# Performance work log

Measured on AMD Instinct MI355X. Metric: run time of the kernel, lower is better.

Reference implementation:

```python
import jax, jax.numpy as jnp
import numpy as np

# module hyper-params (from NLSearch __init__ defaults)
K = 7        # top-k neighbors
PS = 7       # patch size
WS = 8       # search window (ws x ws candidates)
NHEADS = 1
STRIDE0 = 4  # query grid stride
STRIDE1 = 1  # candidate stride within window


def _reflect(i, n):
    # reflect (mirror) out-of-range indices into [0, n)
    i = jnp.where(i < 0, -i, i)
    return jnp.where(i >= n, 2 * (n - 1) - i, i)


def setup_inputs() -> dict:
    key = jax.random.key(0)
    k0, k1 = jax.random.split(key)
    vid0 = jax.random.normal(k0, (1, 3, 32, 256, 256), dtype=jnp.float32)
    vid1 = jax.random.normal(k1, (1, 3, 32, 256, 256), dtype=jnp.float32)
    return {"vid0": vid0, "vid1": vid1}


def _nl_search(vid0, vid1):
    B, T, C, H, W = vid0.shape
    HD = NHEADS
    c = C // HD
    v0 = vid0.reshape(B, T, HD, c, H, W)
    v1 = vid1.reshape(B, T, HD, c, H, W)
    nH = (H - 1) // STRIDE0 + 1
    nW = (W - 1) // STRIDE0 + 1
    qh = jnp.arange(nH) * STRIDE0  # query centers
    qw = jnp.arange(nW) * STRIDE0
    poff = jnp.arange(PS) - PS // 2  # centered patch offsets

    def patches(v, hc, wc):
        # gather reflect-bounded ps x ps patches centered at (hc, wc)
        hi = _reflect(hc[:, None] + poff[None, :], H)  # [nH, PS]
        wi = _reflect(wc[:, None] + poff[None, :], W)  # [nW, PS]
        p = v[:, :, :, :, hi]          # [B,T,HD,c,nH,PS,W]
        p = p[:, :, :, :, :, :, wi]    # [B,T,HD,c,nH,PS,nW,PS]
        return p

    p0 = patches(v0, qh, qw)  # query patches, reused across all shifts
    woff = (jnp.arange(WS) - WS // 2) * STRIDE1
    shifts = jnp.stack(jnp.meshgrid(woff, woff, indexing='ij'), -1).reshape(-1, 2)  # [WS*WS,2]

    def body(carry, s):
        def step(s_):
            p1 = patches(v1, qh + s_[0], qw + s_[1])
            # patch inner product ('prod' search distance)
            return jnp.einsum('bthcnivj,bthcnivj->bthnv', p0, p1)
        return carry, jax.checkpoint(step)(s)

    _, dists = jax.lax.scan(body, 0, shifts)   # [L,B,T,HD,nH,nW]
    dists = jnp.moveaxis(dists, 0, -1)         # [B,T,HD,nH,nW,L]

    # anchor_self: force the self (zero-shift) candidate to rank first,
    # but return its true distance (bump only used for ordering)
    self_idx = (WS // 2) * WS + (WS // 2)
    adj = dists.at[..., self_idx].add(jnp.asarray(1e30, dists.dtype))
    _, top_idx = jax.lax.top_k(adj, K)                       # [B,T,HD,nH,nW,K]
    top_d = jnp.take_along_axis(dists, top_idx, axis=-1)     # [B,T,HD,nH,nW,K]

    # decode flat shift index -> absolute (t,h,w) neighbor coordinates
    dh = (top_idx // WS - WS // 2) * STRIDE1
    dw = (top_idx % WS - WS // 2) * STRIDE1
    hh = _reflect(qh[None, None, None, :, None, None] + dh, H)
    ww = _reflect(qw[None, None, None, None, :, None] + dw, W)
    tt = jnp.broadcast_to(jnp.arange(T)[None, :, None, None, None, None], hh.shape)
    inds = jnp.stack([tt, hh, ww], -1)  # [B,T,HD,nH,nW,K,3]

    Q = T * nH * nW
    dists_out = jnp.transpose(top_d, (0, 2, 1, 3, 4, 5)).reshape(B, HD, Q, K)
    inds_out = jnp.transpose(inds, (0, 2, 1, 3, 4, 5, 6)).reshape(B, HD, Q, K, 3)
    return dists_out, inds_out


def reference(vid0, vid1):
    return _nl_search(vid0, vid1)
```

## Files before the change

### kernel.cpp

```cpp
#include <hip/hip_runtime.h>

#define TT 3
#define CCH 32
#define HH 256
#define WW 256
#define KK 7
#define NQ 64
#define QPB 16
#define V1W 80
#define V1N (14*V1W)
#define V1P (V1N + 8)
#define V0W 72
#define V0N (7*V0W)
#define V0P (V0N + 16)
#define CHC 4

__device__ __forceinline__ int refl(int i, int n) {
    i = i < 0 ? -i : i;
    return i >= n ? 2*(n-1) - i : i;
}

__global__ __launch_bounds__(256, 4)
void nls_kernel(const float* __restrict__ vid0, const float* __restrict__ vid1,
                float* __restrict__ out) {
    __shared__ float v1s[CHC * V1P];
    __shared__ float v0s[CHC * V0P];

    const int bx  = blockIdx.x;
    const int t   = bx >> 8;
    const int rem = bx & 255;
    const int qy  = rem >> 2;
    const int q0  = (rem & 3) * QPB;
    const int qh  = qy * 4;
    const int w0  = 4*q0 - 7;

    const int tid   = threadIdx.x;
    const int qwi   = tid & 15;
    const int clane = (tid >> 4) & 3;
    const int shq   = tid >> 6;

    int off1[5];
#pragma unroll
    for (int k = 0; k < 5; ++k) {
        int idx = tid + 256*k;
        if (idx < V1N) {
            int r = idx / V1W, wi = idx - r*V1W;
            off1[k] = refl(qh + r - 7, HH) * WW + refl(w0 + wi, WW);
        } else off1[k] = 0;
    }
    int off0[2];
#pragma unroll
    for (int k = 0; k < 2; ++k) {
        int idx = tid + 256*k;
        if (idx < V0N) {
            int r = idx / V0W, wi = idx - r*V0W;
            off0[k] = refl(qh + r - 3, HH) * WW + refl(w0 + wi, WW);
        } else off0[k] = 0;
    }

    float acc[2][8];
#pragma unroll
    for (int l = 0; l < 2; ++l)
#pragma unroll
        for (int b = 0; b < 8; ++b) acc[l][b] = 0.f;

    const float* g0 = vid0 + (size_t)t * (CCH*HH*WW);
    const float* g1 = vid1 + (size_t)t * (CCH*HH*WW);

#pragma unroll 1
    for (int s = 0; s < 8; ++s) {
        const int cb = CHC * s * (HH*WW);
        __syncthreads();
        float t1[CHC][5];
        float t0v[CHC][2];
#pragma unroll
        for (int ch = 0; ch < CHC; ++ch) {
            const float* p1 = g1 + cb + ch*(HH*WW);
            const float* p0 = g0 + cb + ch*(HH*WW);
#pragma unroll
            for (int k = 0; k < 4; ++k) t1[ch][k] = p1[off1[k]];
            t1[ch][4]  = (tid < V1N - 1024) ? p1[off1[4]] : 0.f;
            t0v[ch][0] = p0[off0[0]];
            t0v[ch][1] = (tid < V0N - 256) ? p0[off0[1]] : 0.f;
        }
#pragma unroll
        for (int ch = 0; ch < CHC; ++ch) {
#pragma unroll
            for (int k = 0; k < 4; ++k) v1s[ch*V1P + tid + 256*k] = t1[ch][k];
            if (tid < V1N - 1024) v1s[ch*V1P + tid + 1024] = t1[ch][4];
            v0s[ch*V0P + tid] = t0v[ch][0];
            if (tid < V0N - 256) v0s[ch*V0P + tid + 256] = t0v[ch][1];
        }
        __syncthreads();

        float x[7][8];
        const float* xb = &v0s[clane*V0P + 4*qwi + 4];
#pragma unroll
        for (int i = 0; i < 7; ++i) {
            float4 a = *(const float4*)(xb + i*V0W);
            float4 b = *(const float4*)(xb + i*V0W + 4);
            x[i][0]=a.x; x[i][1]=a.y; x[i][2]=a.z; x[i][3]=a.w;
            x[i][4]=b.x; x[i][5]=b.y; x[i][6]=b.z; x[i][7]=b.w;
        }
        const float* yb = &v1s[clane*V1P + (2*shq)*V1W + 4*qwi];
#pragma unroll
        for (int rr = 0; rr < 8; ++rr) {
            const float4* py = (const float4*)(yb + rr*V1W);
            float4 A = py[0], B = py[1], C = py[2], D = py[3];
            float y[16];
            y[0]=A.x;  y[1]=A.y;  y[2]=A.z;  y[3]=A.w;
            y[4]=B.x;  y[5]=B.y;  y[6]=B.z;  y[7]=B.w;
            y[8]=C.x;  y[9]=C.y;  y[10]=C.z; y[11]=C.w;
            y[12]=D.x; y[13]=D.y; y[14]=D.z; y[15]=D.w;
            if (rr < 7) {
#pragma unroll
                for (int sw = 0; sw < 8; ++sw)
#pragma unroll
                    for (int j = 0; j < 7; ++j)
                        acc[0][sw] += x[rr][j] * y[sw + j];
            }
            if (rr >= 1) {
#pragma unroll
                for (int sw = 0; sw < 8; ++sw)
#pragma unroll
                    for (int j = 0; j < 7; ++j)
                        acc[1][sw] += x[rr-1][j] * y[sw + j];
            }
        }
    }

#pragma unroll
    for (int m = 16; m <= 32; m <<= 1)
#pragma unroll
        for (int l = 0; l < 2; ++l)
#pragma unroll
            for (int b = 0; b < 8; ++b)
                acc[l][b] += __shfl_xor(acc[l][b], m, 64);

    __syncthreads();
    float* dlds = v1s;
    if (clane == 0) {
#pragma unroll
        for (int l = 0; l < 2; ++l)
#pragma unroll
            for (int b = 0; b < 8; ++b)
                dlds[qwi*64 + (2*shq + l)*8 + b] = acc[l][b];
    }
    __syncthreads();

    {
        const int q16 = tid >> 4;
        const int l16 = tid & 15;
        const float* d = &dlds[q16 * 64];
        const int j0 = l16 * 4;
        float cv[4];
#pragma unroll
        for (int jj = 0; jj < 4; ++jj) {
            float v = d[j0 + jj];
            if (j0 + jj == 36) v += 1e30f;
            cv[jj] = v;
        }
        unsigned mask = 0;
        const int qx = q0 + q16;
        const int q  = (t*NQ + qy)*NQ + qx;
        float* od = out + q*KK;
        float* oi = out + (size_t)TT*NQ*NQ*KK + (size_t)q*KK*3;
        for (int k = 0; k < KK; ++k) {
            float best = -3.4e38f; int bi = 1 << 30;
#pragma unroll
            for (int jj = 0; jj < 4; ++jj)
                if (!(mask & (1u << jj)) && cv[jj] > best) { best = cv[jj]; bi = j0 + jj; }
#pragma unroll
            for (int m = 1; m <= 8; m <<= 1) {
                float ob = __shfl_xor(best, m, 64);
                int  obi = __shfl_xor(bi,  m, 64);
                if (ob > best || (ob == best && obi < bi)) { best = ob; bi = obi; }
            }
            if ((bi >> 2) == l16) mask |= 1u << (bi & 3);
            if (l16 == 0) {
                od[k] = d[bi];
                int dh = (bi >> 3) - 4;
                int dw = (bi & 7) - 4;
                oi[k*3 + 0] = (float)t;
                oi[k*3 + 1] = (float)refl(qh + dh, HH);
                oi[k*3 + 2] = (float)refl(qx*4 + dw, WW);
            }
        }
    }
}

extern "C" void kernel_launch(void* const* d_in, const int* in_sizes, int n_in,
                              void* d_out, int out_size, void* d_ws, size_t ws_size,
                              hipStream_t stream) {
    (void)in_sizes; (void)n_in; (void)d_ws; (void)ws_size; (void)out_size;
    const float* vid0 = (const float*)d_in[0];
    const float* vid1 = (const float*)d_in[1];
    float* out = (float*)d_out;
    nls_kernel<<<dim3(TT * NQ * (NQ / QPB)), dim3(256), 0, stream>>>(vid0, vid1, out);
}
```

Before: 126.6 us.

## Split channel reduction across two blocks and prefetch next chunk into registers

The kernel is split into two launches. In the first, each block handles half of the 32 channels and writes partial distance sums to workspace. In the second, the halves are summed and the top-k selection runs. This doubles the grid from 768 to 1536 blocks for better occupancy on many CUs, and the next chunk's global loads are issued before the compute of the current chunk so that latency overlaps with math. The cost is extra workspace traffic, a second launch, higher register pressure from the prefetch buffers, and a launch-bounds hint raised to 6 waves.

```diff
diff --git a/kernel.cpp b/kernel.cpp
--- a/kernel.cpp
+++ b/kernel.cpp
@@ -14,25 +14,28 @@
 #define V0N (7*V0W)
 #define V0P (V0N + 16)
 #define CHC 4
+#define NCHUNK 4
 
 __device__ __forceinline__ int refl(int i, int n) {
     i = i < 0 ? -i : i;
     return i >= n ? 2*(n-1) - i : i;
 }
 
-__global__ __launch_bounds__(256, 4)
-void nls_kernel(const float* __restrict__ vid0, const float* __restrict__ vid1,
-                float* __restrict__ out) {
+__global__ __launch_bounds__(256, 6)
+void nls_partial(const float* __restrict__ vid0, const float* __restrict__ vid1,
+                 float* __restrict__ ws) {
     __shared__ float v1s[CHC * V1P];
     __shared__ float v0s[CHC * V0P];
 
-    const int bx  = blockIdx.x;
-    const int t   = bx >> 8;
-    const int rem = bx & 255;
-    const int qy  = rem >> 2;
-    const int q0  = (rem & 3) * QPB;
-    const int qh  = qy * 4;
-    const int w0  = 4*q0 - 7;
+    const int bx   = blockIdx.x;
+    const int half = bx & 1;
+    const int b2   = bx >> 1;
+    const int t    = b2 >> 8;
+    const int rem  = b2 & 255;
+    const int qy   = rem >> 2;
+    const int q0   = (rem & 3) * QPB;
+    const int qh   = qy * 4;
+    const int w0   = 4*q0 - 7;
 
     const int tid   = threadIdx.x;
     const int qwi   = tid & 15;
@@ -58,21 +61,20 @@
         } else off0[k] = 0;
     }
 
+    const float* g0 = vid0 + ((size_t)t*CCH + half*16) * (HH*WW);
+    const float* g1 = vid1 + ((size_t)t*CCH + half*16) * (HH*WW);
+
     float acc[2][8];
 #pragma unroll
     for (int l = 0; l < 2; ++l)
 #pragma unroll
         for (int b = 0; b < 8; ++b) acc[l][b] = 0.f;
 
-    const float* g0 = vid0 + (size_t)t * (CCH*HH*WW);
-    const float* g1 = vid1 + (size_t)t * (CCH*HH*WW);
-
-#pragma unroll 1
-    for (int s = 0; s < 8; ++s) {
+    float t1[CHC][5];
+    float t0v[CHC][2];
+
+    auto load_chunk = [&](int s) {
         const int cb = CHC * s * (HH*WW);
-        __syncthreads();
-        float t1[CHC][5];
-        float t0v[CHC][2];
 #pragma unroll
         for (int ch = 0; ch < CHC; ++ch) {
             const float* p1 = g1 + cb + ch*(HH*WW);
@@ -83,6 +85,12 @@
             t0v[ch][0] = p0[off0[0]];
             t0v[ch][1] = (tid < V0N - 256) ? p0[off0[1]] : 0.f;
         }
+    };
+
+    load_chunk(0);
+
+#pragma unroll 1
+    for (int s = 0; s < NCHUNK; ++s) {
 #pragma unroll
         for (int ch = 0; ch < CHC; ++ch) {
 #pragma unroll
@@ -92,6 +100,8 @@
             if (tid < V0N - 256) v0s[ch*V0P + tid + 256] = t0v[ch][1];
         }
         __syncthreads();
+
+        if (s + 1 < NCHUNK) load_chunk(s + 1);
 
         float x[7][8];
         const float* xb = &v0s[clane*V0P + 4*qwi + 4];
@@ -127,6 +137,7 @@
                         acc[1][sw] += x[rr-1][j] * y[sw + j];
             }
         }
+        __syncthreads();
     }
 
 #pragma unroll
@@ -137,7 +148,6 @@
             for (int b = 0; b < 8; ++b)
                 acc[l][b] += __shfl_xor(acc[l][b], m, 64);
 
-    __syncthreads();
     float* dlds = v1s;
     if (clane == 0) {
 #pragma unroll
@@ -148,43 +158,60 @@
     }
     __syncthreads();
 
-    {
-        const int q16 = tid >> 4;
-        const int l16 = tid & 15;
-        const float* d = &dlds[q16 * 64];
-        const int j0 = l16 * 4;
-        float cv[4];
-#pragma unroll
-        for (int jj = 0; jj < 4; ++jj) {
-            float v = d[j0 + jj];
-            if (j0 + jj == 36) v += 1e30f;
-            cv[jj] = v;
-        }
-        unsigned mask = 0;
-        const int qx = q0 + q16;
-        const int q  = (t*NQ + qy)*NQ + qx;
-        float* od = out + q*KK;
-        float* oi = out + (size_t)TT*NQ*NQ*KK + (size_t)q*KK*3;
-        for (int k = 0; k < KK; ++k) {
-            float best = -3.4e38f; int bi = 1 << 30;
-#pragma unroll
-            for (int jj = 0; jj < 4; ++jj)
-                if (!(mask & (1u << jj)) && cv[jj] > best) { best = cv[jj]; bi = j0 + jj; }
-#pragma unroll
-            for (int m = 1; m <= 8; m <<= 1) {
-                float ob = __shfl_xor(best, m, 64);
-                int  obi = __shfl_xor(bi,  m, 64);
-                if (ob > best || (ob == best && obi < bi)) { best = ob; bi = obi; }
-            }
-            if ((bi >> 2) == l16) mask |= 1u << (bi & 3);
-            if (l16 == 0) {
-                od[k] = d[bi];
-                int dh = (bi >> 3) - 4;
-                int dw = (bi & 7) - 4;
-                oi[k*3 + 0] = (float)t;
-                oi[k*3 + 1] = (float)refl(qh + dh, HH);
-                oi[k*3 + 2] = (float)refl(qx*4 + dw, WW);
-            }
+    float* wp = ws + (size_t)bx * 1024;
+    for (int i = tid; i < 1024; i += 256) wp[i] = dlds[i];
+}
+
+__global__ __launch_bounds__(256, 4)
+void nls_topk(const float* __restrict__ ws, float* __restrict__ out) {
+    __shared__ float dlds[QPB * 64];
+    const int p   = blockIdx.x;
+    const int t   = p >> 8;
+    const int rem = p & 255;
+    const int qy  = rem >> 2;
+    const int q0  = (rem & 3) * QPB;
+    const int qh  = qy * 4;
+    const int tid = threadIdx.x;
+
+    const float* a = ws + (size_t)p * 2048;
+    for (int i = tid; i < 1024; i += 256) dlds[i] = a[i] + a[i + 1024];
+    __syncthreads();
+
+    const int q16 = tid >> 4;
+    const int l16 = tid & 15;
+    const float* d = &dlds[q16 * 64];
+    const int j0 = l16 * 4;
+    float cv[4];
+#pragma unroll
+    for (int jj = 0; jj < 4; ++jj) {
+        float v = d[j0 + jj];
+        if (j0 + jj == 36) v += 1e30f;
+        cv[jj] = v;
+    }
+    unsigned mask = 0;
+    const int qx = q0 + q16;
+    const int q  = (t*NQ + qy)*NQ + qx;
+    float* od = out + q*KK;
+    float* oi = out + (size_t)TT*NQ*NQ*KK + (size_t)q*KK*3;
+    for (int k = 0; k < KK; ++k) {
+        float best = -3.4e38f; int bi = 1 << 30;
+#pragma unroll
+        for (int jj = 0; jj < 4; ++jj)
+            if (!(mask & (1u << jj)) && cv[jj] > best) { best = cv[jj]; bi = j0 + jj; }
+#pragma unroll
+        for (int m = 1; m <= 8; m <<= 1) {
+            float ob = __shfl_xor(best, m, 64);
+            int  obi = __shfl_xor(bi,  m, 64);
+            if (ob > best || (ob == best && obi < bi)) { best = ob; bi = obi; }
+        }
+        if ((bi >> 2) == l16) mask |= 1u << (bi & 3);
+        if (l16 == 0) {
+            od[k] = d[bi];
+            int dh = (bi >> 3) - 4;
+            int dw = (bi & 7) - 4;
+            oi[k*3 + 0] = (float)t;
+            oi[k*3 + 1] = (float)refl(qh + dh, HH);
+            oi[k*3 + 2] = (float)refl(qx*4 + dw, WW);
         }
     }
 }
@@ -192,9 +219,11 @@
 extern "C" void kernel_launch(void* const* d_in, const int* in_sizes, int n_in,
                               void* d_out, int out_size, void* d_ws, size_t ws_size,
                               hipStream_t stream) {
-    (void)in_sizes; (void)n_in; (void)d_ws; (void)ws_size; (void)out_size;
+    (void)in_sizes; (void)n_in; (void)ws_size; (void)out_size;
     const float* vid0 = (const float*)d_in[0];
     const float* vid1 = (const float*)d_in[1];
     float* out = (float*)d_out;
-    nls_kernel<<<dim3(TT * NQ * (NQ / QPB)), dim3(256), 0, stream>>>(vid0, vid1, out);
-}
+    float* ws  = (float*)d_ws;
+    nls_partial<<<dim3(2 * TT * NQ * (NQ / QPB)), dim3(256), 0, stream>>>(vid0, vid1, ws);
+    nls_topk<<<dim3(TT * NQ * (NQ / QPB)), dim3(256), 0, stream>>>(ws, out);
+}
```

Measured after the change: 201.3 us. 59.1% more time.

## Load candidate tiles via direct global-to-LDS and read query patches from global

Applied to the files above, without the earlier changes.

Candidate-frame tiles are now copied straight from global memory into LDS with global_load_lds, bypassing registers. The query-patch shared buffer is removed and each thread reads its query rows directly from global into registers. Each chunk now holds 8 channels instead of 4, so there are half as many synchronisation rounds. Threads are regrouped so each covers four shift rows with two channel halves, and the two halves are summed at the end through LDS. The intent is to cut register staging and barrier overhead. In exchange, occupancy drops (launch bounds 3 instead of 4), register pressure rises from 32 accumulators, and the query reads from global are redundant.

```diff
diff --git a/kernel.cpp b/kernel.cpp
--- a/kernel.cpp
+++ b/kernel.cpp
@@ -7,24 +7,28 @@
 #define KK 7
 #define NQ 64
 #define QPB 16
-#define V1W 80
-#define V1N (14*V1W)
-#define V1P (V1N + 8)
-#define V0W 72
-#define V0N (7*V0W)
-#define V0P (V0N + 16)
-#define CHC 4
+#define V1W 76
+#define V1R 14
+#define V1N (V1R*V1W)
+#define V1P 1080
+#define CHC 8
+#define NCHUNK 4
 
 __device__ __forceinline__ int refl(int i, int n) {
     i = i < 0 ? -i : i;
     return i >= n ? 2*(n-1) - i : i;
 }
 
-__global__ __launch_bounds__(256, 4)
+__device__ __forceinline__ void gload_lds(const float* g, float* l) {
+    __builtin_amdgcn_global_load_lds(
+        (const __attribute__((address_space(1))) unsigned int*)g,
+        (__attribute__((address_space(3))) unsigned int*)l, 4, 0, 0);
+}
+
+__global__ __launch_bounds__(256, 3)
 void nls_kernel(const float* __restrict__ vid0, const float* __restrict__ vid1,
                 float* __restrict__ out) {
     __shared__ float v1s[CHC * V1P];
-    __shared__ float v0s[CHC * V0P];
 
     const int bx  = blockIdx.x;
     const int t   = bx >> 8;
@@ -36,8 +40,11 @@
 
     const int tid   = threadIdx.x;
     const int qwi   = tid & 15;
-    const int clane = (tid >> 4) & 3;
-    const int shq   = tid >> 6;
+    const int c01   = (tid >> 4) & 3;
+    const int c2    = (tid >> 6) & 1;
+    const int shh   = tid >> 7;
+    const int clane = c01 + 4*c2;
+    const int qx    = q0 + qwi;
 
     int off1[5];
 #pragma unroll
@@ -48,83 +55,67 @@
             off1[k] = refl(qh + r - 7, HH) * WW + refl(w0 + wi, WW);
         } else off1[k] = 0;
     }
-    int off0[2];
+
+    float acc[4][8];
 #pragma unroll
-    for (int k = 0; k < 2; ++k) {
-        int idx = tid + 256*k;
-        if (idx < V0N) {
-            int r = idx / V0W, wi = idx - r*V0W;
-            off0[k] = refl(qh + r - 3, HH) * WW + refl(w0 + wi, WW);
-        } else off0[k] = 0;
-    }
+    for (int a = 0; a < 4; ++a)
+#pragma unroll
+        for (int b = 0; b < 8; ++b) acc[a][b] = 0.f;
 
-    float acc[2][8];
-#pragma unroll
-    for (int l = 0; l < 2; ++l)
-#pragma unroll
-        for (int b = 0; b < 8; ++b) acc[l][b] = 0.f;
-
-    const float* g0 = vid0 + (size_t)t * (CCH*HH*WW);
-    const float* g1 = vid1 + (size_t)t * (CCH*HH*WW);
+    const float* g0t = vid0 + (size_t)t * (CCH*HH*WW);
+    const float* g1t = vid1 + (size_t)t * (CCH*HH*WW);
 
 #pragma unroll 1
-    for (int s = 0; s < 8; ++s) {
-        const int cb = CHC * s * (HH*WW);
+    for (int s = 0; s < NCHUNK; ++s) {
         __syncthreads();
-        float t1[CHC][5];
-        float t0v[CHC][2];
 #pragma unroll
         for (int ch = 0; ch < CHC; ++ch) {
-            const float* p1 = g1 + cb + ch*(HH*WW);
-            const float* p0 = g0 + cb + ch*(HH*WW);
+            const float* p1 = g1t + (size_t)(CHC*s + ch) * (HH*WW);
+            float* lb = &v1s[ch*V1P + (tid & ~63)];
 #pragma unroll
-            for (int k = 0; k < 4; ++k) t1[ch][k] = p1[off1[k]];
-            t1[ch][4]  = (tid < V1N - 1024) ? p1[off1[4]] : 0.f;
-            t0v[ch][0] = p0[off0[0]];
-            t0v[ch][1] = (tid < V0N - 256) ? p0[off0[1]] : 0.f;
+            for (int k = 0; k < 4; ++k)
+                gload_lds(p1 + off1[k], lb + 256*k);
+            if (tid < V1N - 1024)
+                gload_lds(p1 + off1[4], &v1s[ch*V1P + 1024 + (tid & ~63)]);
         }
+
+        const float* p0 = g0t + (size_t)(CHC*s + clane) * (HH*WW);
+        float x[7][8];
 #pragma unroll
-        for (int ch = 0; ch < CHC; ++ch) {
-#pragma unroll
-            for (int k = 0; k < 4; ++k) v1s[ch*V1P + tid + 256*k] = t1[ch][k];
-            if (tid < V1N - 1024) v1s[ch*V1P + tid + 1024] = t1[ch][4];
-            v0s[ch*V0P + tid] = t0v[ch][0];
-            if (tid < V0N - 256) v0s[ch*V0P + tid + 256] = t0v[ch][1];
+        for (int i = 0; i < 7; ++i) {
+            const float* rowp = p0 + refl(qh + i - 3, HH) * WW;
+            float4 B = *(const float4*)(rowp + 4*qx);
+            float4 A;
+            if (qx > 0) A = *(const float4*)(rowp + 4*qx - 4);
+            else        A = make_float4(0.f, B.w, B.z, B.y);
+            x[i][0]=A.y; x[i][1]=A.z; x[i][2]=A.w;
+            x[i][3]=B.x; x[i][4]=B.y; x[i][5]=B.z; x[i][6]=B.w;
         }
         __syncthreads();
 
-        float x[7][8];
-        const float* xb = &v0s[clane*V0P + 4*qwi + 4];
+        const float* yb = &v1s[clane*V1P + 4*qwi];
 #pragma unroll
-        for (int i = 0; i < 7; ++i) {
-            float4 a = *(const float4*)(xb + i*V0W);
-            float4 b = *(const float4*)(xb + i*V0W + 4);
-            x[i][0]=a.x; x[i][1]=a.y; x[i][2]=a.z; x[i][3]=a.w;
-            x[i][4]=b.x; x[i][5]=b.y; x[i][6]=b.z; x[i][7]=b.w;
-        }
-        const float* yb = &v1s[clane*V1P + (2*shq)*V1W + 4*qwi];
+        for (int rr = 0; rr < 10; ++rr) {
+            const float* yp = yb + (4*shh + rr) * V1W;
+            float4 Ya = ((const float4*)yp)[0];
+            float4 Yb = ((const float4*)yp)[1];
+            float4 Yc = ((const float4*)yp)[2];
+            float4 Yd = ((const float4*)yp)[3];
+            float y[16];
+            y[0]=Ya.x;  y[1]=Ya.y;  y[2]=Ya.z;  y[3]=Ya.w;
+            y[4]=Yb.x;  y[5]=Yb.y;  y[6]=Yb.z;  y[7]=Yb.w;
+            y[8]=Yc.x;  y[9]=Yc.y;  y[10]=Yc.z; y[11]=Yc.w;
+            y[12]=Yd.x; y[13]=Yd.y; y[14]=Yd.z; y[15]=Yd.w;
 #pragma unroll
-        for (int rr = 0; rr < 8; ++rr) {
-            const float4* py = (const float4*)(yb + rr*V1W);
-            float4 A = py[0], B = py[1], C = py[2], D = py[3];
-            float y[16];
-            y[0]=A.x;  y[1]=A.y;  y[2]=A.z;  y[3]=A.w;
-            y[4]=B.x;  y[5]=B.y;  y[6]=B.z;  y[7]=B.w;
-            y[8]=C.x;  y[9]=C.y;  y[10]=C.z; y[11]=C.w;
-            y[12]=D.x; y[13]=D.y; y[14]=D.z; y[15]=D.w;
-            if (rr < 7) {
+            for (int a = 0; a < 4; ++a) {
+                const int pi = rr - a;
+                if (pi >= 0 && pi < 7) {
 #pragma unroll
-                for (int sw = 0; sw < 8; ++sw)
+                    for (int sw = 0; sw < 8; ++sw)
 #pragma unroll
-                    for (int j = 0; j < 7; ++j)
-                        acc[0][sw] += x[rr][j] * y[sw + j];
-            }
-            if (rr >= 1) {
-#pragma unroll
-                for (int sw = 0; sw < 8; ++sw)
-#pragma unroll
-                    for (int j = 0; j < 7; ++j)
-                        acc[1][sw] += x[rr-1][j] * y[sw + j];
+                        for (int j = 0; j < 7; ++j)
+                            acc[a][sw] += x[pi][j] * y[sw + j];
+                }
             }
         }
     }
@@ -132,37 +123,39 @@
 #pragma unroll
     for (int m = 16; m <= 32; m <<= 1)
 #pragma unroll
-        for (int l = 0; l < 2; ++l)
+        for (int a = 0; a < 4; ++a)
 #pragma unroll
             for (int b = 0; b < 8; ++b)
-                acc[l][b] += __shfl_xor(acc[l][b], m, 64);
+                acc[a][b] += __shfl_xor(acc[a][b], m, 64);
 
     __syncthreads();
     float* dlds = v1s;
-    if (clane == 0) {
+    if (c01 == 0) {
 #pragma unroll
-        for (int l = 0; l < 2; ++l)
-#pragma unroll
-            for (int b = 0; b < 8; ++b)
-                dlds[qwi*64 + (2*shq + l)*8 + b] = acc[l][b];
+        for (int a = 0; a < 4; ++a) {
+            float* dp = &dlds[c2*1024 + qwi*64 + (shh*4 + a)*8];
+            *(float4*)(dp)     = make_float4(acc[a][0], acc[a][1], acc[a][2], acc[a][3]);
+            *(float4*)(dp + 4) = make_float4(acc[a][4], acc[a][5], acc[a][6], acc[a][7]);
+        }
     }
     __syncthreads();
 
     {
         const int q16 = tid >> 4;
         const int l16 = tid & 15;
-        const float* d = &dlds[q16 * 64];
+        const float* d0 = &dlds[q16 * 64];
+        const float* d1 = d0 + 1024;
         const int j0 = l16 * 4;
         float cv[4];
 #pragma unroll
         for (int jj = 0; jj < 4; ++jj) {
-            float v = d[j0 + jj];
+            float v = d0[j0 + jj] + d1[j0 + jj];
             if (j0 + jj == 36) v += 1e30f;
             cv[jj] = v;
         }
         unsigned mask = 0;
-        const int qx = q0 + q16;
-        const int q  = (t*NQ + qy)*NQ + qx;
+        const int qxx = q0 + q16;
+        const int q   = (t*NQ + qy)*NQ + qxx;
         float* od = out + q*KK;
         float* oi = out + (size_t)TT*NQ*NQ*KK + (size_t)q*KK*3;
         for (int k = 0; k < KK; ++k) {
@@ -178,12 +171,12 @@
             }
             if ((bi >> 2) == l16) mask |= 1u << (bi & 3);
             if (l16 == 0) {
-                od[k] = d[bi];
+                od[k] = d0[bi] + d1[bi];
                 int dh = (bi >> 3) - 4;
                 int dw = (bi & 7) - 4;
                 oi[k*3 + 0] = (float)t;
                 oi[k*3 + 1] = (float)refl(qh + dh, HH);
-                oi[k*3 + 2] = (float)refl(qx*4 + dw, WW);
+                oi[k*3 + 2] = (float)refl(qxx*4 + dw, WW);
             }
         }
     }
```

New measurement: 124.4 us. About the same (-1.7%).
